# Optimization experiments

Measured on AMD Instinct MI355X. Metric: run time of the kernel, lower is better.

Reference implementation:

```python
import jax, jax.numpy as jnp
import numpy as np

SMOOTH = 4.0

def setup_inputs() -> dict:
    key = jax.random.key(0)
    k1, k2, k3, k4 = jax.random.split(key, 4)
    B, Na, Nb, Dk, Dim = 256, 196, 196, 256, 1024
    return {
        "query_a": jax.random.normal(k1, (B, Na, Dk), dtype=jnp.float32),
        "value_a": jax.random.normal(k2, (B, Dim, Na), dtype=jnp.float32),
        "key_b": jax.random.normal(k3, (B, Dk, Nb), dtype=jnp.float32),
        "value_b": jax.random.normal(k4, (B, Dim, Nb), dtype=jnp.float32),
        "gamma": jnp.zeros((1,), dtype=jnp.float32),
    }

def reference(query_a, value_a, key_b, value_b, gamma):
    # energy: [B, Na, Nb]
    energy = jnp.einsum("bak,bkn->ban", query_a, key_b)
    attn = jax.nn.softmax(energy * SMOOTH, axis=-1)
    # output: [B, dim, Nb]
    out = jnp.einsum("bda,ban->bdn", value_a, attn)
    return gamma + out + value_b
```

## Files before the change

### kernel.cpp

```cpp
#include <hip/hip_runtime.h>
#include <stdint.h>

#define NBATCH 256
#define NA 196
#define NB 196
#define DK 256
#define DIM 1024
#define SM_C 5.770780163555854f

#define NT 13
#define AW 13
#define KSTR 40
#define PSTR 232
#define KROWS 208
#define PROWS 208

typedef short short8 __attribute__((ext_vector_type(8)));
typedef float floatx4 __attribute__((ext_vector_type(4)));
typedef float f4 __attribute__((ext_vector_type(4)));

__device__ __forceinline__ unsigned short f32_bf16(float f) {
    unsigned u = __builtin_bit_cast(unsigned, f);
    u += 0x7fffu + ((u >> 16) & 1u);
    return (unsigned short)(u >> 16);
}
__device__ __forceinline__ float bf16_f32(unsigned short h) {
    return __builtin_bit_cast(float, (unsigned)h << 16);
}

__global__ __launch_bounds__(1024, 4) void xattn_fused(
    const float* __restrict__ Q,
    const float* __restrict__ Kg,
    const float* __restrict__ Va,
    const float* __restrict__ Vb,
    const float* __restrict__ gamma,
    float* __restrict__ Out)
{
    const int b = blockIdx.x;
    const float* Qb  = Q  + (size_t)b * NA * DK;
    const float* Kb  = Kg + (size_t)b * DK * NB;
    const float* VAb = Va + (size_t)b * DIM * NA;
    const float* VBb = Vb + (size_t)b * DIM * NB;
    float*       Ob  = Out + (size_t)b * DIM * NB;

    __shared__ __align__(16) unsigned short LDSB[PROWS * PSTR];
    unsigned short* KtHi = LDSB;
    unsigned short* KtLo = LDSB + KROWS * KSTR;
    unsigned short* Pl   = LDSB;

    const int tid  = threadIdx.x;
    const int wave = tid >> 6;
    const int lane = tid & 63;
    const int q    = lane >> 4;
    const int lm   = lane & 15;

    for (int it = tid; it < KROWS * KSTR; it += 1024)
        ((unsigned*)LDSB)[it] = 0;

    floatx4 acc[NT];
#pragma unroll
    for (int nt = 0; nt < NT; ++nt) acc[nt] = (floatx4){0.f, 0.f, 0.f, 0.f};

    const int aw = wave * 16 + lm;
    const int aq = aw < NA ? aw : NA - 1;
    const float* qrow = Qb + (size_t)aq * DK;

    for (int kc = 0; kc < 8; ++kc) {
        const int k0 = kc * 32;
        f4 qv0, qv1;
        if (wave < AW) {
            qv0 = *(const f4*)(qrow + k0 + q * 8);
            qv1 = *(const f4*)(qrow + k0 + q * 8 + 4);
        }
        __syncthreads();
        for (int it = tid; it < 32 * 49; it += 1024) {
            const int kk = it / 49;
            const int n4 = (it % 49) * 4;
            const f4 v = *(const f4*)(Kb + (size_t)(k0 + kk) * NB + n4);
#pragma unroll
            for (int j = 0; j < 4; ++j) {
                const float f = v[j];
                const unsigned short hi = f32_bf16(f);
                KtHi[(n4 + j) * KSTR + kk] = hi;
                KtLo[(n4 + j) * KSTR + kk] = f32_bf16(f - bf16_f32(hi));
            }
        }
        __syncthreads();
        if (wave < AW) {
            short8 qHi, qLo;
#pragma unroll
            for (int j = 0; j < 8; ++j) {
                const float f = (j < 4) ? qv0[j] : qv1[j - 4];
                const unsigned short hi = f32_bf16(f);
                qHi[j] = (short)hi;
                qLo[j] = (short)f32_bf16(f - bf16_f32(hi));
            }
#pragma unroll
            for (int nt = 0; nt < NT; ++nt) {
                const short8 kHi = *(const short8*)&KtHi[(nt * 16 + lm) * KSTR + q * 8];
                const short8 kLo = *(const short8*)&KtLo[(nt * 16 + lm) * KSTR + q * 8];
                acc[nt] = __builtin_amdgcn_mfma_f32_16x16x32_bf16(kHi, qHi, acc[nt], 0, 0, 0);
                acc[nt] = __builtin_amdgcn_mfma_f32_16x16x32_bf16(kLo, qHi, acc[nt], 0, 0, 0);
                acc[nt] = __builtin_amdgcn_mfma_f32_16x16x32_bf16(kHi, qLo, acc[nt], 0, 0, 0);
            }
        }
    }

    float inv = 0.f;
    if (wave < AW) {
        float m = -3.0e38f;
#pragma unroll
        for (int nt = 0; nt < NT; ++nt)
#pragma unroll
            for (int r = 0; r < 4; ++r) {
                const int n = nt * 16 + q * 4 + r;
                if (n < NB) m = fmaxf(m, acc[nt][r]);
            }
        m = fmaxf(m, __shfl_xor(m, 16));
        m = fmaxf(m, __shfl_xor(m, 32));
        float s = 0.f;
#pragma unroll
        for (int nt = 0; nt < NT; ++nt)
#pragma unroll
            for (int r = 0; r < 4; ++r) {
                const int n = nt * 16 + q * 4 + r;
                const float p = (n < NB) ? exp2f((acc[nt][r] - m) * SM_C) : 0.f;
                acc[nt][r] = p;
                s += p;
            }
        s += __shfl_xor(s, 16);
        s += __shfl_xor(s, 32);
        inv = 1.f / s;
    }

    __syncthreads();
    for (int it = tid; it < (PROWS * PSTR) / 2; it += 1024)
        ((unsigned*)LDSB)[it] = 0;
    __syncthreads();
    if (wave < AW && aw < NA) {
#pragma unroll
        for (int nt = 0; nt < NT; ++nt)
#pragma unroll
            for (int r = 0; r < 4; ++r) {
                const int n = nt * 16 + q * 4 + r;
                if (n < NB)
                    Pl[(size_t)n * PSTR + aw] = f32_bf16(acc[nt][r] * inv);
            }
    }
    __syncthreads();

    const float g = gamma[0];
#pragma unroll 1
    for (int pass = 0; pass < 4; ++pass) {
        const int dbase = pass * 256 + wave * 16;
        const float* varow = VAb + (size_t)(dbase + lm) * NA;
        floatx4 o[NT];
#pragma unroll
        for (int nt = 0; nt < NT; ++nt) o[nt] = (floatx4){0.f, 0.f, 0.f, 0.f};

        for (int ac = 0; ac < 7; ++ac) {
            const int a0 = ac * 32 + q * 8;
            short8 aF;
            if (ac < 6) {
                const f4 v0 = *(const f4*)(varow + a0);
                const f4 v1 = *(const f4*)(varow + a0 + 4);
#pragma unroll
                for (int j = 0; j < 8; ++j)
                    aF[j] = (short)f32_bf16((j < 4) ? v0[j] : v1[j - 4]);
            } else {
#pragma unroll
                for (int j = 0; j < 8; ++j) {
                    int a = a0 + j;
                    a = a < NA ? a : NA - 1;
                    aF[j] = (short)f32_bf16(varow[a]);
                }
            }
#pragma unroll
            for (int nt = 0; nt < NT; ++nt) {
                const short8 bF = *(const short8*)&Pl[(size_t)(nt * 16 + lm) * PSTR + ac * 32 + q * 8];
                o[nt] = __builtin_amdgcn_mfma_f32_16x16x32_bf16(aF, bF, o[nt], 0, 0, 0);
            }
        }

#pragma unroll
        for (int nt = 0; nt < NT; ++nt) {
            const int n = nt * 16 + lm;
            if (n < NB) {
#pragma unroll
                for (int r = 0; r < 4; ++r) {
                    const size_t off = (size_t)(dbase + q * 4 + r) * NB + n;
                    Ob[off] = o[nt][r] + VBb[off] + g;
                }
            }
        }
    }
}

extern "C" void kernel_launch(void* const* d_in, const int* in_sizes, int n_in,
                              void* d_out, int out_size, void* d_ws, size_t ws_size,
                              hipStream_t stream) {
    const float* Q  = (const float*)d_in[0];
    const float* VA = (const float*)d_in[1];
    const float* KB = (const float*)d_in[2];
    const float* VB = (const float*)d_in[3];
    const float* GM = (const float*)d_in[4];
    float* out = (float*)d_out;
    xattn_fused<<<NBATCH, 1024, 0, stream>>>(Q, KB, VA, VB, GM, out);
}
```

Before: 588.8 us.

## Double-buffer K tiles in LDS and prefetch Q and Va fragments

The energy-phase K staging now uses two LDS buffers. The next K chunk and Q fragment are loaded from global memory before the current chunk's MFMAs run, and written to LDS afterwards, which removes one barrier per iteration. The K stride changes to 42, so fragments are read with 32-bit loads, presumably to cut LDS bank conflicts. The value_a loop is fully unrolled with a one-step register prefetch, and the clamped tail load is replaced by clamped vector loads. This raises register pressure under a 1024-thread launch bound and uses narrower LDS reads.

```diff
diff --git a/kernel.cpp b/kernel.cpp
--- a/kernel.cpp
+++ b/kernel.cpp
@@ -10,14 +10,16 @@
 
 #define NT 13
 #define AW 13
-#define KSTR 40
+#define KSTR 42
+#define KROWS 208
+#define KBUF (KROWS * KSTR)
 #define PSTR 232
-#define KROWS 208
 #define PROWS 208
 
 typedef short short8 __attribute__((ext_vector_type(8)));
 typedef float floatx4 __attribute__((ext_vector_type(4)));
 typedef float f4 __attribute__((ext_vector_type(4)));
+typedef unsigned uint4v __attribute__((ext_vector_type(4)));
 
 __device__ __forceinline__ unsigned short f32_bf16(float f) {
     unsigned u = __builtin_bit_cast(unsigned, f);
@@ -26,6 +28,15 @@
 }
 __device__ __forceinline__ float bf16_f32(unsigned short h) {
     return __builtin_bit_cast(float, (unsigned)h << 16);
+}
+
+__device__ __forceinline__ short8 frag16(const unsigned short* p) {
+    uint4v u;
+    u[0] = *(const unsigned*)(p + 0);
+    u[1] = *(const unsigned*)(p + 2);
+    u[2] = *(const unsigned*)(p + 4);
+    u[3] = *(const unsigned*)(p + 6);
+    return __builtin_bit_cast(short8, u);
 }
 
 __global__ __launch_bounds__(1024, 4) void xattn_fused(
@@ -44,9 +55,7 @@
     float*       Ob  = Out + (size_t)b * DIM * NB;
 
     __shared__ __align__(16) unsigned short LDSB[PROWS * PSTR];
-    unsigned short* KtHi = LDSB;
-    unsigned short* KtLo = LDSB + KROWS * KSTR;
-    unsigned short* Pl   = LDSB;
+    unsigned short* Pl = LDSB;
 
     const int tid  = threadIdx.x;
     const int wave = tid >> 6;
@@ -54,7 +63,7 @@
     const int q    = lane >> 4;
     const int lm   = lane & 15;
 
-    for (int it = tid; it < KROWS * KSTR; it += 1024)
+    for (int it = tid; it < 2 * KBUF; it += 1024)
         ((unsigned*)LDSB)[it] = 0;
 
     floatx4 acc[NT];
@@ -65,27 +74,69 @@
     const int aq = aw < NA ? aw : NA - 1;
     const float* qrow = Qb + (size_t)aq * DK;
 
+    auto sload = [&](int k0, f4* sv) {
+        {
+            const int kk = tid / 49, n4 = (tid % 49) * 4;
+            sv[0] = *(const f4*)(Kb + (size_t)(k0 + kk) * NB + n4);
+        }
+        if (tid < 544) {
+            const int it = tid + 1024;
+            const int kk = it / 49, n4 = (it % 49) * 4;
+            sv[1] = *(const f4*)(Kb + (size_t)(k0 + kk) * NB + n4);
+        }
+    };
+    auto swrite = [&](unsigned short* Hi, unsigned short* Lo, const f4* sv) {
+        {
+            const int kk = tid / 49, n4 = (tid % 49) * 4;
+#pragma unroll
+            for (int j = 0; j < 4; ++j) {
+                const float f = sv[0][j];
+                const unsigned short hi = f32_bf16(f);
+                Hi[(n4 + j) * KSTR + kk] = hi;
+                Lo[(n4 + j) * KSTR + kk] = f32_bf16(f - bf16_f32(hi));
+            }
+        }
+        if (tid < 544) {
+            const int it = tid + 1024;
+            const int kk = it / 49, n4 = (it % 49) * 4;
+#pragma unroll
+            for (int j = 0; j < 4; ++j) {
+                const float f = sv[1][j];
+                const unsigned short hi = f32_bf16(f);
+                Hi[(n4 + j) * KSTR + kk] = hi;
+                Lo[(n4 + j) * KSTR + kk] = f32_bf16(f - bf16_f32(hi));
+            }
+        }
+    };
+
+    {
+        f4 sv[2];
+        sload(0, sv);
+        swrite(LDSB, LDSB + KBUF, sv);
+    }
+    f4 qv0, qv1;
+    if (wave < AW) {
+        qv0 = *(const f4*)(qrow + q * 8);
+        qv1 = *(const f4*)(qrow + q * 8 + 4);
+    }
+    __syncthreads();
+
+#pragma unroll 1
     for (int kc = 0; kc < 8; ++kc) {
-        const int k0 = kc * 32;
-        f4 qv0, qv1;
-        if (wave < AW) {
-            qv0 = *(const f4*)(qrow + k0 + q * 8);
-            qv1 = *(const f4*)(qrow + k0 + q * 8 + 4);
-        }
-        __syncthreads();
-        for (int it = tid; it < 32 * 49; it += 1024) {
-            const int kk = it / 49;
-            const int n4 = (it % 49) * 4;
-            const f4 v = *(const f4*)(Kb + (size_t)(k0 + kk) * NB + n4);
-#pragma unroll
-            for (int j = 0; j < 4; ++j) {
-                const float f = v[j];
-                const unsigned short hi = f32_bf16(f);
-                KtHi[(n4 + j) * KSTR + kk] = hi;
-                KtLo[(n4 + j) * KSTR + kk] = f32_bf16(f - bf16_f32(hi));
-            }
-        }
-        __syncthreads();
+        unsigned short* HiC = (kc & 1) ? (LDSB + 2 * KBUF) : LDSB;
+        unsigned short* LoC = HiC + KBUF;
+        unsigned short* HiN = (kc & 1) ? LDSB : (LDSB + 2 * KBUF);
+        unsigned short* LoN = HiN + KBUF;
+
+        f4 sv[2];
+        if (kc < 7) sload((kc + 1) * 32, sv);
+
+        f4 qn0, qn1;
+        if (wave < AW && kc < 7) {
+            qn0 = *(const f4*)(qrow + (kc + 1) * 32 + q * 8);
+            qn1 = *(const f4*)(qrow + (kc + 1) * 32 + q * 8 + 4);
+        }
+
         if (wave < AW) {
             short8 qHi, qLo;
 #pragma unroll
@@ -97,13 +148,20 @@
             }
 #pragma unroll
             for (int nt = 0; nt < NT; ++nt) {
-                const short8 kHi = *(const short8*)&KtHi[(nt * 16 + lm) * KSTR + q * 8];
-                const short8 kLo = *(const short8*)&KtLo[(nt * 16 + lm) * KSTR + q * 8];
+                const int ro = (nt * 16 + lm) * KSTR + q * 8;
+                const short8 kHi = frag16(HiC + ro);
+                const short8 kLo = frag16(LoC + ro);
                 acc[nt] = __builtin_amdgcn_mfma_f32_16x16x32_bf16(kHi, qHi, acc[nt], 0, 0, 0);
                 acc[nt] = __builtin_amdgcn_mfma_f32_16x16x32_bf16(kLo, qHi, acc[nt], 0, 0, 0);
                 acc[nt] = __builtin_amdgcn_mfma_f32_16x16x32_bf16(kHi, qLo, acc[nt], 0, 0, 0);
             }
         }
+
+        if (kc < 7) {
+            swrite(HiN, LoN, sv);
+            if (wave < AW) { qv0 = qn0; qv1 = qn1; }
+        }
+        __syncthreads();
     }
 
     float inv = 0.f;
@@ -133,7 +191,6 @@
         inv = 1.f / s;
     }
 
-    __syncthreads();
     for (int it = tid; it < (PROWS * PSTR) / 2; it += 1024)
         ((unsigned*)LDSB)[it] = 0;
     __syncthreads();
@@ -158,28 +215,27 @@
 #pragma unroll
         for (int nt = 0; nt < NT; ++nt) o[nt] = (floatx4){0.f, 0.f, 0.f, 0.f};
 
+        f4 c0 = *(const f4*)(varow + q * 8);
+        f4 c1 = *(const f4*)(varow + q * 8 + 4);
+
+#pragma unroll
         for (int ac = 0; ac < 7; ++ac) {
-            const int a0 = ac * 32 + q * 8;
+            f4 n0, n1;
+            if (ac < 6) {
+                const int a0 = (ac + 1) * 32 + q * 8;
+                n0 = *(const f4*)(varow + (a0     <= 192 ? a0     : 192));
+                n1 = *(const f4*)(varow + (a0 + 4 <= 192 ? a0 + 4 : 192));
+            }
             short8 aF;
-            if (ac < 6) {
-                const f4 v0 = *(const f4*)(varow + a0);
-                const f4 v1 = *(const f4*)(varow + a0 + 4);
-#pragma unroll
-                for (int j = 0; j < 8; ++j)
-                    aF[j] = (short)f32_bf16((j < 4) ? v0[j] : v1[j - 4]);
-            } else {
-#pragma unroll
-                for (int j = 0; j < 8; ++j) {
-                    int a = a0 + j;
-                    a = a < NA ? a : NA - 1;
-                    aF[j] = (short)f32_bf16(varow[a]);
-                }
-            }
+#pragma unroll
+            for (int j = 0; j < 8; ++j)
+                aF[j] = (short)f32_bf16((j < 4) ? c0[j] : c1[j - 4]);
 #pragma unroll
             for (int nt = 0; nt < NT; ++nt) {
                 const short8 bF = *(const short8*)&Pl[(size_t)(nt * 16 + lm) * PSTR + ac * 32 + q * 8];
                 o[nt] = __builtin_amdgcn_mfma_f32_16x16x32_bf16(aF, bF, o[nt], 0, 0, 0);
             }
+            if (ac < 6) { c0 = n0; c1 = n1; }
         }
 
 #pragma unroll
```

After: 586.6 us. No clear change (-0.4%).
